# Kernel optimization log

Measured on AMD Instinct MI355X. Metric: run time of the kernel, lower is better.

## Reference

```python
import jax, jax.numpy as jnp
import numpy as np

N = 50000       # nodes
E = 1600000     # edges
G = 16          # graphs in batch
NUMCHIP = 16    # node features
NUMEDGE = 8     # edge features
H = 32          # hidden_channels
NEG = 0.2       # LeakyReLU slope (PyG GAT default)


def _wegat_conv(x, ea, src, dst, Wn, bn, We, be, att):
    """Edge-weighted GAT conv: returns (node_out [N,H], edge_out [E,NUMEDGE])."""
    xn = x @ Wn + bn                      # [N, H]
    ea2 = ea @ We + be                    # [E, NUMEDGE]
    xi = xn[dst]                          # [E, H] target features
    xj = xn[src]                          # [E, H] source features
    logits = jnp.concatenate([xi, xj, ea2], axis=-1) @ att   # [E]
    logits = jax.nn.leaky_relu(logits, NEG)
    # numerically stable softmax over incoming edges per destination node
    m = jax.ops.segment_max(logits, dst, num_segments=N)
    m = jnp.where(jnp.isfinite(m), m, 0.0)
    p = jnp.exp(logits - m[dst])
    s = jax.ops.segment_sum(p, dst, num_segments=N)
    alpha = p / (s[dst] + 1e-16)          # [E]
    out = jax.ops.segment_sum(xj * alpha[:, None], dst, num_segments=N)  # [N, H]
    return out, ea2


def setup_inputs() -> dict:
    key = jax.random.key(0)
    ks = jax.random.split(key, 24)

    def gl(k, shape):
        fan_in = shape[0] if len(shape) > 1 else shape[0]
        return jax.random.normal(k, shape, dtype=jnp.float32) * (1.0 / np.sqrt(fan_in))

    inp = {
        'x': jax.random.normal(ks[0], (N, NUMCHIP), dtype=jnp.float32),
        'edge_attr': jax.random.normal(ks[1], (E, NUMEDGE), dtype=jnp.float32),
        'edge_index': jax.random.randint(ks[2], (2, E), 0, N, dtype=jnp.int64),
        'batch': jnp.sort(jax.random.randint(ks[3], (N,), 0, G, dtype=jnp.int64)),
        # layer 1
        'Wn1': gl(ks[4], (NUMCHIP, H)), 'bn1': jnp.zeros((H,), jnp.float32),
        'We1': gl(ks[5], (NUMEDGE, NUMEDGE)), 'be1': jnp.zeros((NUMEDGE,), jnp.float32),
        'att1': gl(ks[6], (2 * H + NUMEDGE,)),
        # layer 2
        'Wn2': gl(ks[7], (H, H)), 'bn2': jnp.zeros((H,), jnp.float32),
        'We2': gl(ks[8], (NUMEDGE, NUMEDGE)), 'be2': jnp.zeros((NUMEDGE,), jnp.float32),
        'att2': gl(ks[9], (2 * H + NUMEDGE,)),
        # layer 3
        'Wn3': gl(ks[10], (H, H)), 'bn3': jnp.zeros((H,), jnp.float32),
        'We3': gl(ks[11], (NUMEDGE, NUMEDGE)), 'be3': jnp.zeros((NUMEDGE,), jnp.float32),
        'att3': gl(ks[12], (2 * H + NUMEDGE,)),
        # head
        'Wlin': gl(ks[13], (H, 1)), 'blin': jnp.zeros((1,), jnp.float32),
    }
    return inp


def reference(x, edge_attr, edge_index, batch,
              Wn1, bn1, We1, be1, att1,
              Wn2, bn2, We2, be2, att2,
              Wn3, bn3, We3, be3, att3,
              Wlin, blin):
    src, dst = edge_index[0], edge_index[1]
    x1, ea1 = _wegat_conv(x, edge_attr, src, dst, Wn1, bn1, We1, be1, att1)
    x1 = jax.nn.relu(x1)  # NOTE: original's edge_attr.relu() is a discarded no-op
    x2, ea2 = _wegat_conv(x1, ea1, src, dst, Wn2, bn2, We2, be2, att2)
    x2 = jax.nn.relu(x2)
    x3, _ = _wegat_conv(x2, ea2, src, dst, Wn3, bn3, We3, be3, att3)
    # global mean pool over graphs
    sums = jax.ops.segment_sum(x3, batch, num_segments=G)                   # [G, H]
    cnts = jax.ops.segment_sum(jnp.ones((N,), x3.dtype), batch, num_segments=G)
    pooled = sums / jnp.maximum(cnts, 1.0)[:, None]
    return pooled @ Wlin + blin  # [G, 1]
```

## Files before the change

### kernel.cpp

```cpp
#include <hip/hip_runtime.h>
#include <math.h>


__global__ __launch_bounds__(256) void hist_kernel(const int* __restrict__ dst, int* cnt, int E) {
    int e = blockIdx.x * blockDim.x + threadIdx.x;
    if (e < E) atomicAdd(&cnt[dst[e]], 1);
}

__global__ __launch_bounds__(1024) void scan_kernel(const int* __restrict__ cnt,
                                                    int* rowptr, int* cursor, int n) {
    __shared__ int sums[1024];
    int t = threadIdx.x;
    int CH = (n + 1023) >> 10;
    int s0 = t * CH;
    int s1 = min(n, s0 + CH);
    int local = 0;
    for (int i = s0; i < s1; i++) local += cnt[i];
    sums[t] = local;
    __syncthreads();
    for (int off = 1; off < 1024; off <<= 1) {
        int v = (t >= off) ? sums[t - off] : 0;
        __syncthreads();
        sums[t] += v;
        __syncthreads();
    }
    int run = (t == 0) ? 0 : sums[t - 1];
    for (int i = s0; i < s1; i++) {
        rowptr[i] = run;
        cursor[i] = run;
        run += cnt[i];
    }
    if (t == 1023) rowptr[n] = sums[1023];
}

__global__ __launch_bounds__(256) void scatter_kernel(const int* __restrict__ src,
                                                      const int* __restrict__ dst,
                                                      int* cursor, int2* __restrict__ pack, int E) {
    int e = blockIdx.x * blockDim.x + threadIdx.x;
    if (e >= E) return;
    int d = dst[e];
    int pos = atomicAdd(&cursor[d], 1);
    pack[pos] = make_int2(src[e], e);
}

template <int IN>
__global__ __launch_bounds__(256) void node_linear(const float* __restrict__ xin,
                                                   const float* __restrict__ Wn,
                                                   const float* __restrict__ bn,
                                                   const float* __restrict__ att,
                                                   float* __restrict__ xn,
                                                   float* __restrict__ ai,
                                                   float* __restrict__ aj, int n) {
    int t = blockIdx.x * blockDim.x + threadIdx.x;
    int node = t >> 5;
    int h = t & 31;
    if (node >= n) return;
    float acc = bn[h];
#pragma unroll
    for (int k = 0; k < IN; k++) {
        acc = fmaf(xin[node * IN + k], Wn[k * 32 + h], acc);
    }
    xn[node * 32 + h] = acc;
    float pi = acc * att[h];
    float pj = acc * att[32 + h];
#pragma unroll
    for (int off = 16; off > 0; off >>= 1) {
        pi += __shfl_xor(pi, off);
        pj += __shfl_xor(pj, off);
    }
    if (h == 0) {
        ai[node] = pi;
        aj[node] = pj;
    }
}

__global__ __launch_bounds__(256) void edge_chain(
    const float* __restrict__ ein,
    const float* __restrict__ We1, const float* __restrict__ be1, const float* __restrict__ a1,
    const float* __restrict__ We2, const float* __restrict__ be2, const float* __restrict__ a2,
    const float* __restrict__ We3, const float* __restrict__ be3, const float* __restrict__ a3,
    float* __restrict__ ae1, float* __restrict__ ae2, float* __restrict__ ae3, int E) {
    int e = blockIdx.x * blockDim.x + threadIdx.x;
    if (e >= E) return;
    const float4* p = (const float4*)(ein + (size_t)e * 8);
    float4 x0 = p[0], x1 = p[1];
    float v[8] = {x0.x, x0.y, x0.z, x0.w, x1.x, x1.y, x1.z, x1.w};
    float t[8], u[8];
    float d1 = 0.f, d2 = 0.f, d3 = 0.f;
#pragma unroll
    for (int j = 0; j < 8; j++) {
        float a = be1[j];
#pragma unroll
        for (int k = 0; k < 8; k++) a = fmaf(v[k], We1[k * 8 + j], a);
        t[j] = a;
        d1 = fmaf(a, a1[j], d1);
    }
#pragma unroll
    for (int j = 0; j < 8; j++) {
        float a = be2[j];
#pragma unroll
        for (int k = 0; k < 8; k++) a = fmaf(t[k], We2[k * 8 + j], a);
        u[j] = a;
        d2 = fmaf(a, a2[j], d2);
    }
#pragma unroll
    for (int j = 0; j < 8; j++) {
        float a = be3[j];
#pragma unroll
        for (int k = 0; k < 8; k++) a = fmaf(u[k], We3[k * 8 + j], a);
        d3 = fmaf(a, a3[j], d3);
    }
    ae1[e] = d1;
    ae2[e] = d2;
    ae3[e] = d3;
}

__global__ __launch_bounds__(256) void gat_aggregate(const float* __restrict__ xn,
                                                     const float* __restrict__ ai,
                                                     const float* __restrict__ aj,
                                                     const float* __restrict__ ae,
                                                     const int* __restrict__ rowptr,
                                                     const int2* __restrict__ pack,
                                                     float* __restrict__ xout,
                                                     int n, int relu_out) {
    int wave = (blockIdx.x * blockDim.x + threadIdx.x) >> 6;
    int lane = threadIdx.x & 63;
    if (wave >= n) return;
    int node = wave;
    int row = rowptr[node];
    int deg = rowptr[node + 1] - row;
    int h = lane & 31;
    if (deg == 0) {
        if (lane < 32) xout[node * 32 + h] = 0.f;
        return;
    }
    float a_i = ai[node];
    const int2* pk = pack + row;
    int half = lane >> 5;

    if (deg <= 64) {
        int s = 0;
        float lg = 0.f;
        bool act = (lane < deg);
        if (act) {
            int2 q = pk[lane];
            s = q.x;
            lg = a_i + aj[s] + ae[q.y];
            lg = (lg >= 0.f) ? lg : 0.2f * lg;
        }
        float mx = act ? lg : -INFINITY;
#pragma unroll
        for (int off = 32; off > 0; off >>= 1) mx = fmaxf(mx, __shfl_xor(mx, off));
        float p = act ? expf(lg - mx) : 0.f;
        float psum = p;
#pragma unroll
        for (int off = 32; off > 0; off >>= 1) psum += __shfl_xor(psum, off);
        float acc = 0.f;
        int csize = deg;
        for (int j = half; j < csize; j += 2) {
            float pj = __shfl(p, j);
            int sj = __shfl(s, j);
            acc = fmaf(pj, xn[sj * 32 + h], acc);
        }
        acc += __shfl_xor(acc, 32);
        float o = acc / (psum + 1e-16f);
        if (relu_out) o = fmaxf(o, 0.f);
        if (lane < 32) xout[node * 32 + h] = o;
        return;
    }

    float mx = -INFINITY;
    for (int k = lane; k < deg; k += 64) {
        int2 q = pk[k];
        float lg = a_i + aj[q.x] + ae[q.y];
        lg = (lg >= 0.f) ? lg : 0.2f * lg;
        mx = fmaxf(mx, lg);
    }
#pragma unroll
    for (int off = 32; off > 0; off >>= 1) mx = fmaxf(mx, __shfl_xor(mx, off));

    float acc = 0.f, psum = 0.f;
    for (int base = 0; base < deg; base += 64) {
        int k = base + lane;
        float p = 0.f;
        int s = 0;
        if (k < deg) {
            int2 q = pk[k];
            s = q.x;
            float lg = a_i + aj[s] + ae[q.y];
            lg = (lg >= 0.f) ? lg : 0.2f * lg;
            p = expf(lg - mx);
        }
        psum += p;
        int csize = min(64, deg - base);
        for (int j = half; j < csize; j += 2) {
            float pj = __shfl(p, j);
            int sj = __shfl(s, j);
            acc = fmaf(pj, xn[sj * 32 + h], acc);
        }
    }
#pragma unroll
    for (int off = 32; off > 0; off >>= 1) psum += __shfl_xor(psum, off);
    acc += __shfl_xor(acc, 32);

    float o = acc / (psum + 1e-16f);
    if (relu_out) o = fmaxf(o, 0.f);
    if (lane < 32) xout[node * 32 + h] = o;
}

__global__ __launch_bounds__(256) void pool_kernel(const float* __restrict__ x3,
                                                   const int* __restrict__ batch,
                                                   float* pool, int n) {
    int h = threadIdx.x & 31;
    int rowl = threadIdx.x >> 5;
    int per = (n + gridDim.x - 1) / gridDim.x;
    int n0 = blockIdx.x * per;
    int n1 = min(n, n0 + per);
    float acc = 0.f;
    int curg = -1;
    for (int i = n0 + rowl; i < n1; i += 8) {
        int g = batch[i];
        if (g != curg) {
            if (curg >= 0) atomicAdd(&pool[curg * 32 + h], acc);
            acc = 0.f;
            curg = g;
        }
        acc += x3[i * 32 + h];
    }
    if (curg >= 0) atomicAdd(&pool[curg * 32 + h], acc);
}

__global__ __launch_bounds__(64) void head_kernel(const float* __restrict__ pool,
                                                  const int* __restrict__ batch,
                                                  const float* __restrict__ Wlin,
                                                  const float* __restrict__ blin,
                                                  float* out, int n, int G) {
    int g = threadIdx.x;
    if (g >= G) return;
    float s = 0.f;
#pragma unroll
    for (int k = 0; k < 32; k++) s = fmaf(pool[g * 32 + k], Wlin[k], s);
    int lo = 0, hi = n;
    while (lo < hi) {
        int m = (lo + hi) >> 1;
        if (batch[m] < g) lo = m + 1; else hi = m;
    }
    int start = lo;
    lo = 0; hi = n;
    while (lo < hi) {
        int m = (lo + hi) >> 1;
        if (batch[m] < g + 1) lo = m + 1; else hi = m;
    }
    float c = fmaxf((float)(lo - start), 1.f);
    out[g] = s / c + blin[0];
}

extern "C" void kernel_launch(void* const* d_in, const int* in_sizes, int n_in,
                              void* d_out, int out_size, void* d_ws, size_t ws_size,
                              hipStream_t stream) {
    const float* x    = (const float*)d_in[0];
    const float* ea0  = (const float*)d_in[1];
    const int* ei     = (const int*)d_in[2];
    const int* batch  = (const int*)d_in[3];
    const float* Wn[3] = {(const float*)d_in[4], (const float*)d_in[9],  (const float*)d_in[14]};
    const float* bn[3] = {(const float*)d_in[5], (const float*)d_in[10], (const float*)d_in[15]};
    const float* We[3] = {(const float*)d_in[6], (const float*)d_in[11], (const float*)d_in[16]};
    const float* be[3] = {(const float*)d_in[7], (const float*)d_in[12], (const float*)d_in[17]};
    const float* att[3]= {(const float*)d_in[8], (const float*)d_in[13], (const float*)d_in[18]};
    const float* Wlin = (const float*)d_in[19];
    const float* blin = (const float*)d_in[20];
    float* out = (float*)d_out;

    const int N = in_sizes[0] / 16;
    const int E = in_sizes[1] / 8;
    const int G = out_size;
    (void)n_in; (void)ws_size;

    const int* srcp = ei;
    const int* dstp = ei + E;

    char* base = (char*)d_ws;
    size_t off = 0;
    auto carve = [&](size_t bytes) -> void* {
        void* p = base + off;
        off = (off + bytes + 255) & ~(size_t)255;
        return p;
    };
    float* xnA   = (float*)carve((size_t)N * 32 * 4);
    float* xnB   = (float*)carve((size_t)N * 32 * 4);
    float* ai    = (float*)carve((size_t)N * 4);
    float* aj    = (float*)carve((size_t)N * 4);
    float* ae1   = (float*)carve((size_t)E * 4);
    float* ae2   = (float*)carve((size_t)E * 4);
    float* ae3   = (float*)carve((size_t)E * 4);
    int* cnt     = (int*)carve((size_t)N * 4);
    int* rowptr  = (int*)carve((size_t)(N + 1) * 4);
    int* cursor  = (int*)carve((size_t)N * 4);
    int2* pack   = (int2*)carve((size_t)E * 8);
    float* pool  = (float*)carve((size_t)G * 32 * 4);

    int ebks = (E + 255) / 256;
    int nhbks = (N * 32 + 255) / 256;
    int aggbks = (N + 3) / 4;

    hipMemsetAsync(cnt, 0, (size_t)N * 4, stream);
    hipMemsetAsync(pool, 0, (size_t)G * 32 * 4, stream);
    hist_kernel<<<ebks, 256, 0, stream>>>(dstp, cnt, E);
    scan_kernel<<<1, 1024, 0, stream>>>(cnt, rowptr, cursor, N);
    scatter_kernel<<<ebks, 256, 0, stream>>>(srcp, dstp, cursor, pack, E);

    edge_chain<<<ebks, 256, 0, stream>>>(ea0,
                                         We[0], be[0], att[0] + 64,
                                         We[1], be[1], att[1] + 64,
                                         We[2], be[2], att[2] + 64,
                                         ae1, ae2, ae3, E);

    node_linear<16><<<nhbks, 256, 0, stream>>>(x, Wn[0], bn[0], att[0], xnA, ai, aj, N);
    gat_aggregate<<<aggbks, 256, 0, stream>>>(xnA, ai, aj, ae1, rowptr, pack, xnB, N, 1);

    node_linear<32><<<nhbks, 256, 0, stream>>>(xnB, Wn[1], bn[1], att[1], xnA, ai, aj, N);
    gat_aggregate<<<aggbks, 256, 0, stream>>>(xnA, ai, aj, ae2, rowptr, pack, xnB, N, 1);

    node_linear<32><<<nhbks, 256, 0, stream>>>(xnB, Wn[2], bn[2], att[2], xnA, ai, aj, N);
    gat_aggregate<<<aggbks, 256, 0, stream>>>(xnA, ai, aj, ae3, rowptr, pack, xnB, N, 0);

    pool_kernel<<<128, 256, 0, stream>>>(xnB, batch, pool, N);
    head_kernel<<<1, 64, 0, stream>>>(pool, batch, Wlin, blin, out, N, G);
}
```

Measured before the change: 716.6 us.

## Sort CSR rows by edge id, pre-gather edge logits, serialize aggregation order

Adds a row_sort kernel that bitonic-sorts each destination's incoming edges by original edge id and writes per-row contiguous source indices and per-layer edge attention terms. The aggregation then reads these contiguously instead of gathering through edge ids, normalizes alpha before accumulating, and sums sequentially with non-fused mul/add. This looks aimed at deterministic, reference-matching summation order, though it also removes one indirect gather per layer. It drops the two-half lane split, so each gather loop now runs a full pass over the edges with half the lanes idle, and adds a one-off sorting pass. Pooling and the head are fused into one kernel with one block per graph, and the serial loop over each graph's nodes in that kernel is slow.

New measurement: 1.469 ms. +105.0%, slower.

```diff
diff --git a/kernel.cpp b/kernel.cpp
--- a/kernel.cpp
+++ b/kernel.cpp
@@ -1,5 +1,6 @@
 #include <hip/hip_runtime.h>
 #include <math.h>
+#include <limits.h>
 
 
 __global__ __launch_bounds__(256) void hist_kernel(const int* __restrict__ dst, int* cnt, int E) {
@@ -79,7 +80,7 @@
     const float* __restrict__ We1, const float* __restrict__ be1, const float* __restrict__ a1,
     const float* __restrict__ We2, const float* __restrict__ be2, const float* __restrict__ a2,
     const float* __restrict__ We3, const float* __restrict__ be3, const float* __restrict__ a3,
-    float* __restrict__ ae1, float* __restrict__ ae2, float* __restrict__ ae3, int E) {
+    float4* __restrict__ aet, int E) {
     int e = blockIdx.x * blockDim.x + threadIdx.x;
     if (e >= E) return;
     const float4* p = (const float4*)(ein + (size_t)e * 8);
@@ -110,17 +111,89 @@
         for (int k = 0; k < 8; k++) a = fmaf(u[k], We3[k * 8 + j], a);
         d3 = fmaf(a, a3[j], d3);
     }
-    ae1[e] = d1;
-    ae2[e] = d2;
-    ae3[e] = d3;
+    aet[e] = make_float4(d1, d2, d3, 0.f);
+}
+
+__global__ __launch_bounds__(256) void row_sort(const int2* __restrict__ pack,
+                                                const int* __restrict__ rowptr,
+                                                const float4* __restrict__ aet,
+                                                int* __restrict__ srcs,
+                                                float* __restrict__ aes1,
+                                                float* __restrict__ aes2,
+                                                float* __restrict__ aes3, int n) {
+    int wave = (blockIdx.x * blockDim.x + threadIdx.x) >> 6;
+    int lane = threadIdx.x & 63;
+    if (wave >= n) return;
+    int row = rowptr[wave];
+    int deg = rowptr[wave + 1] - row;
+    if (deg == 0) return;
+
+    if (deg <= 64) {
+        int e = INT_MAX, s = 0;
+        if (lane < deg) {
+            int2 q = pack[row + lane];
+            s = q.x;
+            e = q.y;
+        }
+#pragma unroll
+        for (int size = 2; size <= 64; size <<= 1) {
+#pragma unroll
+            for (int stride = size >> 1; stride > 0; stride >>= 1) {
+                int pe = __shfl_xor(e, stride);
+                int ps = __shfl_xor(s, stride);
+                bool up = ((lane & size) == 0);
+                bool lower = ((lane & stride) == 0);
+                bool keep = (lower == up) ? (e <= pe) : (e >= pe);
+                e = keep ? e : pe;
+                s = keep ? s : ps;
+            }
+        }
+        if (lane < deg) {
+            srcs[row + lane] = s;
+            float4 a = aet[e];
+            aes1[row + lane] = a.x;
+            aes2[row + lane] = a.y;
+            aes3[row + lane] = a.z;
+        }
+        return;
+    }
+
+    int prev = -1;
+    for (int r = 0; r < deg; r++) {
+        int mn = INT_MAX, ms = 0;
+        for (int k = lane; k < deg; k += 64) {
+            int2 q = pack[row + k];
+            if (q.y > prev && q.y < mn) {
+                mn = q.y;
+                ms = q.x;
+            }
+        }
+#pragma unroll
+        for (int off = 32; off > 0; off >>= 1) {
+            int oe = __shfl_xor(mn, off);
+            int os = __shfl_xor(ms, off);
+            if (oe < mn) {
+                mn = oe;
+                ms = os;
+            }
+        }
+        if (lane == 0) {
+            srcs[row + r] = ms;
+            float4 a = aet[mn];
+            aes1[row + r] = a.x;
+            aes2[row + r] = a.y;
+            aes3[row + r] = a.z;
+        }
+        prev = mn;
+    }
 }
 
 __global__ __launch_bounds__(256) void gat_aggregate(const float* __restrict__ xn,
                                                      const float* __restrict__ ai,
                                                      const float* __restrict__ aj,
-                                                     const float* __restrict__ ae,
+                                                     const float* __restrict__ aes,
                                                      const int* __restrict__ rowptr,
-                                                     const int2* __restrict__ pack,
+                                                     const int* __restrict__ srcs,
                                                      float* __restrict__ xout,
                                                      int n, int relu_out) {
     int wave = (blockIdx.x * blockDim.x + threadIdx.x) >> 6;
@@ -135,35 +208,51 @@
         return;
     }
     float a_i = ai[node];
-    const int2* pk = pack + row;
-    int half = lane >> 5;
+    const int* sp = srcs + row;
+    const float* ap = aes + row;
 
     if (deg <= 64) {
         int s = 0;
-        float lg = 0.f;
+        float lg = -INFINITY;
         bool act = (lane < deg);
         if (act) {
-            int2 q = pk[lane];
-            s = q.x;
-            lg = a_i + aj[s] + ae[q.y];
+            s = sp[lane];
+            lg = a_i + aj[s] + ap[lane];
             lg = (lg >= 0.f) ? lg : 0.2f * lg;
         }
-        float mx = act ? lg : -INFINITY;
+        float mx = lg;
 #pragma unroll
         for (int off = 32; off > 0; off >>= 1) mx = fmaxf(mx, __shfl_xor(mx, off));
         float p = act ? expf(lg - mx) : 0.f;
-        float psum = p;
-#pragma unroll
-        for (int off = 32; off > 0; off >>= 1) psum += __shfl_xor(psum, off);
+        float ps = 0.f;
+        for (int j = 0; j < deg; j++) ps += __shfl(p, j);
+        float al = p / (ps + 1e-16f);
         float acc = 0.f;
-        int csize = deg;
-        for (int j = half; j < csize; j += 2) {
-            float pj = __shfl(p, j);
+        int j = 0;
+        for (; j + 3 < deg; j += 4) {
+            float a0 = __shfl(al, j);
+            int s0 = __shfl(s, j);
+            float a1 = __shfl(al, j + 1);
+            int s1 = __shfl(s, j + 1);
+            float a2 = __shfl(al, j + 2);
+            int s2 = __shfl(s, j + 2);
+            float a3 = __shfl(al, j + 3);
+            int s3 = __shfl(s, j + 3);
+            float g0 = xn[s0 * 32 + h];
+            float g1 = xn[s1 * 32 + h];
+            float g2 = xn[s2 * 32 + h];
+            float g3 = xn[s3 * 32 + h];
+            acc = __fadd_rn(acc, __fmul_rn(a0, g0));
+            acc = __fadd_rn(acc, __fmul_rn(a1, g1));
+            acc = __fadd_rn(acc, __fmul_rn(a2, g2));
+            acc = __fadd_rn(acc, __fmul_rn(a3, g3));
+        }
+        for (; j < deg; j++) {
+            float aj_ = __shfl(al, j);
             int sj = __shfl(s, j);
-            acc = fmaf(pj, xn[sj * 32 + h], acc);
-        }
-        acc += __shfl_xor(acc, 32);
-        float o = acc / (psum + 1e-16f);
+            acc = __fadd_rn(acc, __fmul_rn(aj_, xn[sj * 32 + h]));
+        }
+        float o = acc;
         if (relu_out) o = fmaxf(o, 0.f);
         if (lane < 32) xout[node * 32 + h] = o;
         return;
@@ -171,88 +260,80 @@
 
     float mx = -INFINITY;
     for (int k = lane; k < deg; k += 64) {
-        int2 q = pk[k];
-        float lg = a_i + aj[q.x] + ae[q.y];
+        float lg = a_i + aj[sp[k]] + ap[k];
         lg = (lg >= 0.f) ? lg : 0.2f * lg;
         mx = fmaxf(mx, lg);
     }
 #pragma unroll
     for (int off = 32; off > 0; off >>= 1) mx = fmaxf(mx, __shfl_xor(mx, off));
 
-    float acc = 0.f, psum = 0.f;
+    float ps = 0.f;
+    for (int base = 0; base < deg; base += 64) {
+        int k = base + lane;
+        float p = 0.f;
+        if (k < deg) {
+            float lg = a_i + aj[sp[k]] + ap[k];
+            lg = (lg >= 0.f) ? lg : 0.2f * lg;
+            p = expf(lg - mx);
+        }
+        int csize = min(64, deg - base);
+        for (int j = 0; j < csize; j++) ps += __shfl(p, j);
+    }
+    float denom = ps + 1e-16f;
+    float acc = 0.f;
     for (int base = 0; base < deg; base += 64) {
         int k = base + lane;
         float p = 0.f;
         int s = 0;
         if (k < deg) {
-            int2 q = pk[k];
-            s = q.x;
-            float lg = a_i + aj[s] + ae[q.y];
+            s = sp[k];
+            float lg = a_i + aj[s] + ap[k];
             lg = (lg >= 0.f) ? lg : 0.2f * lg;
             p = expf(lg - mx);
         }
-        psum += p;
+        float al = p / denom;
         int csize = min(64, deg - base);
-        for (int j = half; j < csize; j += 2) {
-            float pj = __shfl(p, j);
+        for (int j = 0; j < csize; j++) {
+            float aj_ = __shfl(al, j);
             int sj = __shfl(s, j);
-            acc = fmaf(pj, xn[sj * 32 + h], acc);
-        }
-    }
-#pragma unroll
-    for (int off = 32; off > 0; off >>= 1) psum += __shfl_xor(psum, off);
-    acc += __shfl_xor(acc, 32);
-
-    float o = acc / (psum + 1e-16f);
+            acc = __fadd_rn(acc, __fmul_rn(aj_, xn[sj * 32 + h]));
+        }
+    }
+    float o = acc;
     if (relu_out) o = fmaxf(o, 0.f);
     if (lane < 32) xout[node * 32 + h] = o;
 }
 
-__global__ __launch_bounds__(256) void pool_kernel(const float* __restrict__ x3,
-                                                   const int* __restrict__ batch,
-                                                   float* pool, int n) {
-    int h = threadIdx.x & 31;
-    int rowl = threadIdx.x >> 5;
-    int per = (n + gridDim.x - 1) / gridDim.x;
-    int n0 = blockIdx.x * per;
-    int n1 = min(n, n0 + per);
-    float acc = 0.f;
-    int curg = -1;
-    for (int i = n0 + rowl; i < n1; i += 8) {
-        int g = batch[i];
-        if (g != curg) {
-            if (curg >= 0) atomicAdd(&pool[curg * 32 + h], acc);
-            acc = 0.f;
-            curg = g;
-        }
-        acc += x3[i * 32 + h];
-    }
-    if (curg >= 0) atomicAdd(&pool[curg * 32 + h], acc);
-}
-
-__global__ __launch_bounds__(64) void head_kernel(const float* __restrict__ pool,
-                                                  const int* __restrict__ batch,
-                                                  const float* __restrict__ Wlin,
-                                                  const float* __restrict__ blin,
-                                                  float* out, int n, int G) {
-    int g = threadIdx.x;
-    if (g >= G) return;
-    float s = 0.f;
-#pragma unroll
-    for (int k = 0; k < 32; k++) s = fmaf(pool[g * 32 + k], Wlin[k], s);
+__global__ __launch_bounds__(64) void poolhead_kernel(const float* __restrict__ x3,
+                                                      const int* __restrict__ batch,
+                                                      const float* __restrict__ Wlin,
+                                                      const float* __restrict__ blin,
+                                                      float* out, int n) {
+    int g = blockIdx.x;
+    int lane = threadIdx.x & 63;
+    int h = lane & 31;
     int lo = 0, hi = n;
     while (lo < hi) {
         int m = (lo + hi) >> 1;
         if (batch[m] < g) lo = m + 1; else hi = m;
     }
     int start = lo;
-    lo = 0; hi = n;
+    lo = start; hi = n;
     while (lo < hi) {
         int m = (lo + hi) >> 1;
         if (batch[m] < g + 1) lo = m + 1; else hi = m;
     }
-    float c = fmaxf((float)(lo - start), 1.f);
-    out[g] = s / c + blin[0];
+    int end = lo;
+    float acc = 0.f;
+    for (int i = start; i < end; i++) acc += x3[i * 32 + h];
+    float c = fmaxf((float)(end - start), 1.f);
+    float pooled = acc / c;
+    float sum = 0.f;
+    for (int k = 0; k < 32; k++) {
+        float v = __shfl(pooled, k);
+        sum = __fadd_rn(sum, __fmul_rn(v, Wlin[k]));
+    }
+    if (lane == 0) out[g] = sum + blin[0];
 }
 
 extern "C" void kernel_launch(void* const* d_in, const int* in_sizes, int n_in,
@@ -274,7 +355,7 @@
     const int N = in_sizes[0] / 16;
     const int E = in_sizes[1] / 8;
     const int G = out_size;
-    (void)n_in; (void)ws_size;
+    (void)n_in; (void)ws_size; (void)G;
 
     const int* srcp = ei;
     const int* dstp = ei + E;
@@ -286,25 +367,27 @@
         off = (off + bytes + 255) & ~(size_t)255;
         return p;
     };
-    float* xnA   = (float*)carve((size_t)N * 32 * 4);
-    float* xnB   = (float*)carve((size_t)N * 32 * 4);
+    float* aes1  = (float*)carve((size_t)E * 4);
+    float* aes2  = (float*)carve((size_t)E * 4);
+    float* aes3  = (float*)carve((size_t)E * 4);
+    int* srcs    = (int*)carve((size_t)E * 4);
     float* ai    = (float*)carve((size_t)N * 4);
     float* aj    = (float*)carve((size_t)N * 4);
-    float* ae1   = (float*)carve((size_t)E * 4);
-    float* ae2   = (float*)carve((size_t)E * 4);
-    float* ae3   = (float*)carve((size_t)E * 4);
     int* cnt     = (int*)carve((size_t)N * 4);
     int* rowptr  = (int*)carve((size_t)(N + 1) * 4);
     int* cursor  = (int*)carve((size_t)N * 4);
     int2* pack   = (int2*)carve((size_t)E * 8);
-    float* pool  = (float*)carve((size_t)G * 32 * 4);
+
+    char* trans = base + off;
+    float4* aet = (float4*)trans;
+    float* xnA  = (float*)trans;
+    float* xnB  = xnA + (size_t)N * 32;
 
     int ebks = (E + 255) / 256;
     int nhbks = (N * 32 + 255) / 256;
     int aggbks = (N + 3) / 4;
 
     hipMemsetAsync(cnt, 0, (size_t)N * 4, stream);
-    hipMemsetAsync(pool, 0, (size_t)G * 32 * 4, stream);
     hist_kernel<<<ebks, 256, 0, stream>>>(dstp, cnt, E);
     scan_kernel<<<1, 1024, 0, stream>>>(cnt, rowptr, cursor, N);
     scatter_kernel<<<ebks, 256, 0, stream>>>(srcp, dstp, cursor, pack, E);
@@ -313,17 +396,19 @@
                                          We[0], be[0], att[0] + 64,
                                          We[1], be[1], att[1] + 64,
                                          We[2], be[2], att[2] + 64,
-                                         ae1, ae2, ae3, E);
+                                         aet, E);
+
+    row_sort<<<aggbks, 256, 0, stream>>>(pack, rowptr, aet,
+                                         srcs, aes1, aes2, aes3, N);
 
     node_linear<16><<<nhbks, 256, 0, stream>>>(x, Wn[0], bn[0], att[0], xnA, ai, aj, N);
-    gat_aggregate<<<aggbks, 256, 0, stream>>>(xnA, ai, aj, ae1, rowptr, pack, xnB, N, 1);
+    gat_aggregate<<<aggbks, 256, 0, stream>>>(xnA, ai, aj, aes1, rowptr, srcs, xnB, N, 1);
 
     node_linear<32><<<nhbks, 256, 0, stream>>>(xnB, Wn[1], bn[1], att[1], xnA, ai, aj, N);
-    gat_aggregate<<<aggbks, 256, 0, stream>>>(xnA, ai, aj, ae2, rowptr, pack, xnB, N, 1);
+    gat_aggregate<<<aggbks, 256, 0, stream>>>(xnA, ai, aj, aes2, rowptr, srcs, xnB, N, 1);
 
     node_linear<32><<<nhbks, 256, 0, stream>>>(xnB, Wn[2], bn[2], att[2], xnA, ai, aj, N);
-    gat_aggregate<<<aggbks, 256, 0, stream>>>(xnA, ai, aj, ae3, rowptr, pack, xnB, N, 0);
-
-    pool_kernel<<<128, 256, 0, stream>>>(xnB, batch, pool, N);
-    head_kernel<<<1, 64, 0, stream>>>(pool, batch, Wlin, blin, out, N, G);
-}
+    gat_aggregate<<<aggbks, 256, 0, stream>>>(xnA, ai, aj, aes3, rowptr, srcs, xnB, N, 0);
+
+    poolhead_kernel<<<G, 64, 0, stream>>>(xnB, batch, Wlin, blin, out, N);
+}
```
